# Kernel optimization log

Measured on AMD Instinct MI355X. Metric: run time of the kernel, lower is better.

## Reference

```python
import jax, jax.numpy as jnp
import numpy as np

E = 4096      # num hyperedges (events)
H1 = 512      # hidden1
H2 = 128      # hidden2 (latent)
NA, NK, NV = 8192, 4096, 1024   # nodes per type: author / keyword / venue
NNZ = 131072  # nonzeros per incidence matrix
SCALE = 0.02  # weight init scale (keeps tanh/exp in sane range)


def setup_inputs() -> dict:
    key = jax.random.key(0)
    ks = iter(jax.random.split(key, 64))
    nrm = lambda shape, s=SCALE: jax.random.normal(next(ks), shape, jnp.float32) * s
    inp = {}
    for t, N in (("a", NA), ("k", NK), ("v", NV)):
        inp["rows_" + t] = jax.random.randint(next(ks), (NNZ,), 0, N, dtype=jnp.int32)
        inp["cols_" + t] = jax.random.randint(next(ks), (NNZ,), 0, E, dtype=jnp.int32)
        inp["vals_" + t] = jax.random.uniform(next(ks), (NNZ,), jnp.float32)
        inp["Wn_" + t] = nrm((E, H1));  inp["bn_" + t] = jnp.zeros((H1,), jnp.float32)
        inp["Wzm_" + t] = nrm((H1, H2)); inp["bzm_" + t] = jnp.zeros((H2,), jnp.float32)
        inp["Wzs_" + t] = nrm((H1, H2)); inp["bzs_" + t] = jnp.zeros((H2,), jnp.float32)
        inp["We_" + t] = nrm((N, H1));  inp["be_" + t] = jnp.zeros((H1,), jnp.float32)
        inp["eps_" + t] = jax.random.normal(next(ks), (N, H2), jnp.float32)
    inp["Watt"] = nrm((H1, H1 // 2)); inp["batt"] = jnp.zeros((H1 // 2,), jnp.float32)
    inp["uatt"] = nrm((H1 // 2,), 0.1)
    inp["Wem"] = nrm((H1, H2)); inp["bem"] = jnp.zeros((H2,), jnp.float32)
    inp["Wes"] = nrm((H1, H2)); inp["bes"] = jnp.zeros((H2,), jnp.float32)
    inp["eps_e"] = jax.random.normal(next(ks), (E, H2), jnp.float32)
    return inp


def _type_branch(rows, cols, vals, N, Wn, bn, Wzm, bzm, Wzs, bzs, We, be, eps):
    # node encoder: tanh(sparse_inc @ Wn + bn);  sparse_inc is [N, E] in COO form
    h = jnp.tanh(jax.ops.segment_sum(vals[:, None] * Wn[cols], rows, num_segments=N) + bn)
    zm = h @ Wzm + bzm
    zs = h @ Wzs + bzs
    z = zm + eps * jnp.exp(zs)          # reparameterization
    # edge encoder: tanh(sparse_inc^T @ We + be) -> [E, H1]
    e = jnp.tanh(jax.ops.segment_sum(vals[:, None] * We[rows], cols, num_segments=E) + be)
    return zm, z, e


def _forward(rows_a, cols_a, vals_a, Wn_a, bn_a, Wzm_a, bzm_a, Wzs_a, bzs_a, We_a, be_a, eps_a,
             rows_k, cols_k, vals_k, Wn_k, bn_k, Wzm_k, bzm_k, Wzs_k, bzs_k, We_k, be_k, eps_k,
             rows_v, cols_v, vals_v, Wn_v, bn_v, Wzm_v, bzm_v, Wzs_v, bzs_v, We_v, be_v, eps_v,
             Watt, batt, uatt, Wem, bem, Wes, bes, eps_e):
    zm_a, z_a, e_a = _type_branch(rows_a, cols_a, vals_a, NA, Wn_a, bn_a, Wzm_a, bzm_a, Wzs_a, bzs_a, We_a, be_a, eps_a)
    zm_k, z_k, e_k = _type_branch(rows_k, cols_k, vals_k, NK, Wn_k, bn_k, Wzm_k, bzm_k, Wzs_k, bzs_k, We_k, be_k, eps_k)
    zm_v, z_v, e_v = _type_branch(rows_v, cols_v, vals_v, NV, Wn_v, bn_v, Wzm_v, bzm_v, Wzs_v, bzs_v, We_v, be_v, eps_v)

    # HyperedgeAttention over node types: [E, T=3, H1]
    edge_embeds = jnp.stack([e_a, e_k, e_v], axis=1)
    u = jnp.tanh(jnp.einsum('eth,hd->etd', edge_embeds, Watt) + batt)
    scores = jnp.einsum('etd,d->et', u, uatt)
    alphas = jax.nn.softmax(scores, axis=1)                  # [E, T]
    edge_embed = jnp.einsum('et,eth->eh', alphas, edge_embeds)  # [E, H1]

    zem = edge_embed @ Wem + bem
    zes = edge_embed @ Wes + bes
    ze = zem + eps_e * jnp.exp(zes)

    # InnerDecoder: z_node @ z_edge^T per type, flattened (sampled and mean variants)
    recon = jnp.concatenate([
        (z_a @ ze.T).ravel(), (z_k @ ze.T).ravel(), (z_v @ ze.T).ravel(),
        (zm_a @ zem.T).ravel(), (zm_k @ zem.T).ravel(), (zm_v @ zem.T).ravel(),
    ])
    return recon


def reference(rows_a, cols_a, vals_a, rows_k, cols_k, vals_k, rows_v, cols_v, vals_v,
              Wn_a, bn_a, Wzm_a, bzm_a, Wzs_a, bzs_a, We_a, be_a, eps_a,
              Wn_k, bn_k, Wzm_k, bzm_k, Wzs_k, bzs_k, We_k, be_k, eps_k,
              Wn_v, bn_v, Wzm_v, bzm_v, Wzs_v, bzs_v, We_v, be_v, eps_v,
              Watt, batt, uatt, Wem, bem, Wes, bes, eps_e):
    return _forward(rows_a, cols_a, vals_a, Wn_a, bn_a, Wzm_a, bzm_a, Wzs_a, bzs_a, We_a, be_a, eps_a,
                    rows_k, cols_k, vals_k, Wn_k, bn_k, Wzm_k, bzm_k, Wzs_k, bzs_k, We_k, be_k, eps_k,
                    rows_v, cols_v, vals_v, Wn_v, bn_v, Wzm_v, bzm_v, Wzs_v, bzs_v, We_v, be_v, eps_v,
                    Watt, batt, uatt, Wem, bem, Wes, bes, eps_e)
```

## Files before the change

### kernel.cpp

```cpp
#include <hip/hip_runtime.h>
#include <hip/hip_bf16.h>

#define NE   4096
#define D1   512
#define D2   128
#define NNZV 131072
#define MTOT 13312

typedef __attribute__((ext_vector_type(8))) short bf16x8;
typedef __attribute__((ext_vector_type(4))) float f32x4;

struct Params {
  const int*   rows[3]; const int* cols[3]; const float* vals[3];
  const float* Wn[3];  const float* bn[3];
  const float* Wzm[3]; const float* bzm[3];
  const float* Wzs[3]; const float* bzs[3];
  const float* We[3];  const float* be[3];
  const float* eps[3];
  const float* Watt; const float* batt; const float* uatt;
  const float* Wem;  const float* bem;  const float* Wes; const float* bes;
  const float* eps_e;
  int* cnt[6]; int* ptr[6]; int* cur[6]; int2* spair[6];
  __hip_bfloat16* Wbf[6];
  __hip_bfloat16* hbf[3];
  __hip_bfloat16* Wzmt[3];
  __hip_bfloat16* Wzst[3];
  float* e[3];
  __hip_bfloat16* Zbf; __hip_bfloat16* Zmbf; __hip_bfloat16* zebf; __hip_bfloat16* zembf;
  float* out;
  int rowbase[3];
  int n8pre[7];
  int ndw;
};

__device__ __forceinline__ float bf2f(short s) {
  return __uint_as_float((unsigned)(unsigned short)s << 16);
}

__device__ __forceinline__ int nseg_of(int sub) {
  if (sub & 1) return NE;
  int t = sub >> 1;
  return t == 0 ? 8192 : (t == 1 ? 4096 : 1024);
}

__global__ void prep_kernel(Params p) {
  int i = blockIdx.x * blockDim.x + threadIdx.x;
  if (i < p.ndw) { ((int*)p.cnt[0])[i] = 0; return; }
  int c = i - p.ndw;
  if (c < p.n8pre[6]) {
    int s = 0;
#pragma unroll
    for (int k = 1; k < 6; ++k) if (c >= p.n8pre[k]) s = k;
    int off8 = c - p.n8pre[s];
    int t = s >> 1;
    const float* src = (s & 1) ? p.We[t] : p.Wn[t];
    __hip_bfloat16* dst = p.Wbf[s];
    const float4 a = *(const float4*)&src[(size_t)off8 * 8];
    const float4 b = *(const float4*)&src[(size_t)off8 * 8 + 4];
    bf16x8 o;
    o[0] = (short)__bfloat16_as_ushort(__float2bfloat16(a.x));
    o[1] = (short)__bfloat16_as_ushort(__float2bfloat16(a.y));
    o[2] = (short)__bfloat16_as_ushort(__float2bfloat16(a.z));
    o[3] = (short)__bfloat16_as_ushort(__float2bfloat16(a.w));
    o[4] = (short)__bfloat16_as_ushort(__float2bfloat16(b.x));
    o[5] = (short)__bfloat16_as_ushort(__float2bfloat16(b.y));
    o[6] = (short)__bfloat16_as_ushort(__float2bfloat16(b.z));
    o[7] = (short)__bfloat16_as_ushort(__float2bfloat16(b.w));
    *(bf16x8*)&dst[(size_t)off8 * 8] = o;
    return;
  }
  int c2 = c - p.n8pre[6];
  if (c2 >= 6 * D1 * D2) return;
  int m = c2 >> 16;
  int e = c2 & 65535;
  int t = m >> 1;
  const float* src = (m & 1) ? p.Wzs[t] : p.Wzm[t];
  __hip_bfloat16* dst = (m & 1) ? p.Wzst[t] : p.Wzmt[t];
  int k = e >> 7, n = e & 127;
  dst[n * D1 + k] = __float2bfloat16(src[e]);
}

__global__ void hist_kernel(Params p) {
  int i = blockIdx.x * blockDim.x + threadIdx.x;
  if (i >= 6 * NNZV) return;
  int sub = i >> 17, idx = i & (NNZV - 1);
  int type = sub >> 1, dir = sub & 1;
  int seg = dir ? p.cols[type][idx] : p.rows[type][idx];
  atomicAdd(&p.cnt[sub][seg], 1);
}

__global__ __launch_bounds__(1024) void scan_kernel(Params p) {
  int sub = blockIdx.x;
  int n = nseg_of(sub);
  const int* cnt = p.cnt[sub];
  int* ptr = p.ptr[sub];
  int* cur = p.cur[sub];
  __shared__ int lds[1024];
  int tid = threadIdx.x;
  int per = (n + 1023) >> 10;
  int base = tid * per;
  int s = 0;
  for (int q = 0; q < per; ++q) { int ix = base + q; if (ix < n) s += cnt[ix]; }
  lds[tid] = s;
  __syncthreads();
  for (int off = 1; off < 1024; off <<= 1) {
    int v = (tid >= off) ? lds[tid - off] : 0;
    __syncthreads();
    lds[tid] += v;
    __syncthreads();
  }
  int prefix = (tid == 0) ? 0 : lds[tid - 1];
  for (int q = 0; q < per; ++q) {
    int ix = base + q;
    if (ix < n) { int c = cnt[ix]; ptr[ix] = prefix; cur[ix] = prefix; prefix += c; }
  }
  if (tid == 1023) ptr[n] = lds[1023];
}

__global__ void scatter_kernel(Params p) {
  int i = blockIdx.x * blockDim.x + threadIdx.x;
  if (i >= 6 * NNZV) return;
  int sub = i >> 17, idx = i & (NNZV - 1);
  int type = sub >> 1, dir = sub & 1;
  int seg = dir ? p.cols[type][idx] : p.rows[type][idx];
  int oth = dir ? p.rows[type][idx] : p.cols[type][idx];
  int pos = atomicAdd(&p.cur[sub][seg], 1);
  p.spair[sub][pos] = make_int2(oth, __float_as_int(p.vals[type][idx]));
}

__global__ __launch_bounds__(128) void spmm_kernel(Params p) {
  int g = blockIdx.x * 2 + (threadIdx.x >> 6);
  int sub, seg;
  if      (g <  8192) { sub = 0; seg = g;         }
  else if (g < 12288) { sub = 1; seg = g - 8192;  }
  else if (g < 16384) { sub = 2; seg = g - 12288; }
  else if (g < 20480) { sub = 3; seg = g - 16384; }
  else if (g < 21504) { sub = 4; seg = g - 20480; }
  else                { sub = 5; seg = g - 21504; }
  int type = sub >> 1, dir = sub & 1;
  const __hip_bfloat16* W = p.Wbf[sub];
  const float* bias = dir ? p.be[type] : p.bn[type];
  const int*  ptr  = p.ptr[sub];
  const int2* pair = p.spair[sub];
  int lane = threadIdx.x & 63;
  int c0 = lane * 8;
  float acc[8];
#pragma unroll
  for (int j = 0; j < 8; ++j) acc[j] = 0.f;
  int q0 = ptr[seg], q1 = ptr[seg + 1];
  int q = q0;
  for (; q + 4 <= q1; q += 4) {
    int2 pr0 = pair[q], pr1 = pair[q + 1], pr2 = pair[q + 2], pr3 = pair[q + 3];
    const bf16x8 w0 = *(const bf16x8*)(W + (size_t)pr0.x * D1 + c0);
    const bf16x8 w1 = *(const bf16x8*)(W + (size_t)pr1.x * D1 + c0);
    const bf16x8 w2 = *(const bf16x8*)(W + (size_t)pr2.x * D1 + c0);
    const bf16x8 w3 = *(const bf16x8*)(W + (size_t)pr3.x * D1 + c0);
    float v0 = __int_as_float(pr0.y), v1 = __int_as_float(pr1.y);
    float v2 = __int_as_float(pr2.y), v3 = __int_as_float(pr3.y);
#pragma unroll
    for (int j = 0; j < 8; ++j)
      acc[j] += v0 * bf2f(w0[j]) + v1 * bf2f(w1[j]) + v2 * bf2f(w2[j]) + v3 * bf2f(w3[j]);
  }
  for (; q < q1; ++q) {
    int2 pr = pair[q];
    const bf16x8 wv = *(const bf16x8*)(W + (size_t)pr.x * D1 + c0);
    float v = __int_as_float(pr.y);
#pragma unroll
    for (int j = 0; j < 8; ++j) acc[j] += v * bf2f(wv[j]);
  }
  const float4 b0 = *(const float4*)&bias[c0];
  const float4 b1 = *(const float4*)&bias[c0 + 4];
  float r[8];
  r[0] = tanhf(acc[0] + b0.x); r[1] = tanhf(acc[1] + b0.y);
  r[2] = tanhf(acc[2] + b0.z); r[3] = tanhf(acc[3] + b0.w);
  r[4] = tanhf(acc[4] + b1.x); r[5] = tanhf(acc[5] + b1.y);
  r[6] = tanhf(acc[6] + b1.z); r[7] = tanhf(acc[7] + b1.w);
  if (dir) {
    float4 o0 = {r[0], r[1], r[2], r[3]};
    float4 o1 = {r[4], r[5], r[6], r[7]};
    *(float4*)&p.e[type][(size_t)seg * D1 + c0]     = o0;
    *(float4*)&p.e[type][(size_t)seg * D1 + c0 + 4] = o1;
  } else {
    bf16x8 ob;
#pragma unroll
    for (int j = 0; j < 8; ++j) ob[j] = (short)__bfloat16_as_ushort(__float2bfloat16(r[j]));
    *(bf16x8*)&p.hbf[type][(size_t)seg * D1 + c0] = ob;
  }
}

__global__ __launch_bounds__(128) void zmzs_kernel(Params p) {
  int b = blockIdx.x;
  int type, blk;
  if      (b < 256) { type = 0; blk = b;       }
  else if (b < 384) { type = 1; blk = b - 256; }
  else              { type = 2; blk = b - 384; }
  int row0 = blk * 32;
  const __hip_bfloat16* A  = p.hbf[type];
  const __hip_bfloat16* Bm = p.Wzmt[type];
  const __hip_bfloat16* Bs = p.Wzst[type];
  int wid = threadIdx.x >> 6, lane = threadIdx.x & 63;
  int rloc = lane & 15, kg = lane >> 4;
  int mrow = row0 + wid * 16 + rloc;
  f32x4 accm[8], accs[8];
  f32x4 zero = {0.f, 0.f, 0.f, 0.f};
#pragma unroll
  for (int nf = 0; nf < 8; ++nf) { accm[nf] = zero; accs[nf] = zero; }
  for (int kk = 0; kk < 16; ++kk) {
    bf16x8 a = *(const bf16x8*)(A + (size_t)mrow * D1 + kk * 32 + kg * 8);
#pragma unroll
    for (int nf = 0; nf < 8; ++nf) {
      int ncol = nf * 16 + rloc;
      bf16x8 bm = *(const bf16x8*)(Bm + (size_t)ncol * D1 + kk * 32 + kg * 8);
      accm[nf] = __builtin_amdgcn_mfma_f32_16x16x32_bf16(a, bm, accm[nf], 0, 0, 0);
      bf16x8 bs = *(const bf16x8*)(Bs + (size_t)ncol * D1 + kk * 32 + kg * 8);
      accs[nf] = __builtin_amdgcn_mfma_f32_16x16x32_bf16(a, bs, accs[nf], 0, 0, 0);
    }
  }
  int base = p.rowbase[type];
  const float* eps = p.eps[type];
  const float* bzm = p.bzm[type];
  const float* bzs = p.bzs[type];
  int rbase = row0 + wid * 16 + kg * 4;
#pragma unroll
  for (int nf = 0; nf < 8; ++nf) {
    int col = nf * 16 + rloc;
    float bm = bzm[col], bs = bzs[col];
#pragma unroll
    for (int jj = 0; jj < 4; ++jj) {
      int row = rbase + jj;
      float zm = accm[nf][jj] + bm;
      float zs = accs[nf][jj] + bs;
      float ep = eps[(size_t)row * D2 + col];
      float z  = zm + ep * expf(zs);
      size_t oi = (size_t)(base + row) * D2 + col;
      p.Zmbf[oi] = __float2bfloat16(zm);
      p.Zbf[oi]  = __float2bfloat16(z);
    }
  }
}

__global__ __launch_bounds__(256) void scorecomb_kernel(Params p) {
  __shared__ __align__(16) float em[24 * D1];
  __shared__ float sc[24];
  __shared__ float alpha[8][3];
  int e0 = blockIdx.x * 8;
  int tid = threadIdx.x;
  for (int i4 = tid; i4 < 24 * (D1 / 4); i4 += 256) {
    int r = i4 >> 7, h4 = i4 & 127;
    int el = r / 3, t = r - el * 3;
    ((float4*)em)[i4] = ((const float4*)(p.e[t] + (size_t)(e0 + el) * D1))[h4];
  }
  __syncthreads();
  int lane = tid & 63, w = tid >> 6;
  {
    int d0 = lane * 4;
    float acc[6][4];
#pragma unroll
    for (int r = 0; r < 6; ++r) { acc[r][0]=acc[r][1]=acc[r][2]=acc[r][3]=0.f; }
    for (int hh = 0; hh < D1; hh += 4) {
      float4 w0 = *(const float4*)&p.Watt[(size_t)(hh+0) * 256 + d0];
      float4 w1 = *(const float4*)&p.Watt[(size_t)(hh+1) * 256 + d0];
      float4 w2 = *(const float4*)&p.Watt[(size_t)(hh+2) * 256 + d0];
      float4 w3 = *(const float4*)&p.Watt[(size_t)(hh+3) * 256 + d0];
#pragma unroll
      for (int r = 0; r < 6; ++r) {
        const float4 ev = *(const float4*)&em[(w * 6 + r) * D1 + hh];
        acc[r][0] += ev.x*w0.x + ev.y*w1.x + ev.z*w2.x + ev.w*w3.x;
        acc[r][1] += ev.x*w0.y + ev.y*w1.y + ev.z*w2.y + ev.w*w3.y;
        acc[r][2] += ev.x*w0.z + ev.y*w1.z + ev.z*w2.z + ev.w*w3.z;
        acc[r][3] += ev.x*w0.w + ev.y*w1.w + ev.z*w2.w + ev.w*w3.w;
      }
    }
    const float4 u4 = *(const float4*)&p.uatt[d0];
    const float4 b4 = *(const float4*)&p.batt[d0];
#pragma unroll
    for (int r = 0; r < 6; ++r) {
      float s = u4.x * tanhf(acc[r][0] + b4.x) + u4.y * tanhf(acc[r][1] + b4.y)
              + u4.z * tanhf(acc[r][2] + b4.z) + u4.w * tanhf(acc[r][3] + b4.w);
#pragma unroll
      for (int off = 32; off > 0; off >>= 1) s += __shfl_down(s, off, 64);
      if (lane == 0) sc[w * 6 + r] = s;
    }
  }
  __syncthreads();
  if (tid < 8) {
    float s0 = sc[tid * 3 + 0], s1 = sc[tid * 3 + 1], s2 = sc[tid * 3 + 2];
    float m = fmaxf(s0, fmaxf(s1, s2));
    float a0 = expf(s0 - m), a1 = expf(s1 - m), a2 = expf(s2 - m);
    float inv = 1.f / (a0 + a1 + a2);
    alpha[tid][0] = a0 * inv; alpha[tid][1] = a1 * inv; alpha[tid][2] = a2 * inv;
  }
  __syncthreads();
  float4 ve[4];
#pragma unroll
  for (int k = 0; k < 4; ++k) {
    int i4 = tid + k * 256;
    int el = i4 >> 7, h4 = i4 & 127;
    float4 va = ((const float4*)em)[(el * 3 + 0) * 128 + h4];
    float4 vk = ((const float4*)em)[(el * 3 + 1) * 128 + h4];
    float4 vv = ((const float4*)em)[(el * 3 + 2) * 128 + h4];
    float a0 = alpha[el][0], a1 = alpha[el][1], a2 = alpha[el][2];
    ve[k].x = a0*va.x + a1*vk.x + a2*vv.x;
    ve[k].y = a0*va.y + a1*vk.y + a2*vv.y;
    ve[k].z = a0*va.z + a1*vk.z + a2*vv.z;
    ve[k].w = a0*va.w + a1*vk.w + a2*vv.w;
  }
  __syncthreads();
#pragma unroll
  for (int k = 0; k < 4; ++k)
    ((float4*)em)[tid + k * 256] = ve[k];
  __syncthreads();
  int jp = tid & 63, eg = tid >> 6;
  int j = jp * 2;
  float am[2][2], as[2][2];
#pragma unroll
  for (int r = 0; r < 2; ++r) { am[r][0]=am[r][1]=as[r][0]=as[r][1]=0.f; }
  for (int hh = 0; hh < D1; hh += 4) {
    float2 wm[4], ws[4];
#pragma unroll
    for (int q = 0; q < 4; ++q) {
      wm[q] = *(const float2*)&p.Wem[(size_t)(hh + q) * D2 + j];
      ws[q] = *(const float2*)&p.Wes[(size_t)(hh + q) * D2 + j];
    }
#pragma unroll
    for (int r = 0; r < 2; ++r) {
      const float4 ev = *(const float4*)&em[(eg * 2 + r) * D1 + hh];
      am[r][0] += ev.x*wm[0].x + ev.y*wm[1].x + ev.z*wm[2].x + ev.w*wm[3].x;
      am[r][1] += ev.x*wm[0].y + ev.y*wm[1].y + ev.z*wm[2].y + ev.w*wm[3].y;
      as[r][0] += ev.x*ws[0].x + ev.y*ws[1].x + ev.z*ws[2].x + ev.w*ws[3].x;
      as[r][1] += ev.x*ws[0].y + ev.y*ws[1].y + ev.z*ws[2].y + ev.w*ws[3].y;
    }
  }
  float bm0 = p.bem[j], bm1 = p.bem[j+1], bs0 = p.bes[j], bs1 = p.bes[j+1];
#pragma unroll
  for (int r = 0; r < 2; ++r) {
    int e = e0 + eg * 2 + r;
    float zm0 = am[r][0] + bm0, zm1 = am[r][1] + bm1;
    float zs0 = as[r][0] + bs0, zs1 = as[r][1] + bs1;
    float e0v = p.eps_e[(size_t)e * D2 + j], e1v = p.eps_e[(size_t)e * D2 + j + 1];
    float z0 = zm0 + e0v * expf(zs0), z1 = zm1 + e1v * expf(zs1);
    size_t oi = (size_t)e * D2 + j;
    p.zembf[oi]   = __float2bfloat16(zm0); p.zembf[oi+1] = __float2bfloat16(zm1);
    p.zebf[oi]    = __float2bfloat16(z0);  p.zebf[oi+1]  = __float2bfloat16(z1);
  }
}

#define DT_N 128
__global__ __launch_bounds__(256) void decode_kernel(Params p) {
  __shared__ __align__(16) float cs[64][DT_N + 4];
  int which = blockIdx.z;
  const __hip_bfloat16* A = which ? p.Zmbf  : p.Zbf;
  const __hip_bfloat16* B = which ? p.zembf : p.zebf;
  float* C = p.out + (size_t)which * MTOT * NE;
  int n0 = blockIdx.x * DT_N;
  int m0 = blockIdx.y * 64;
  int wid  = threadIdx.x >> 6;
  int lane = threadIdx.x & 63;
  int rloc = lane & 15;
  int kg   = lane >> 4;
  int mrow = m0 + wid * 16 + rloc;
  bf16x8 a[4];
#pragma unroll
  for (int kk = 0; kk < 4; ++kk)
    a[kk] = *(const bf16x8*)(A + (size_t)mrow * D2 + kk * 32 + kg * 8);
  f32x4 acc[DT_N / 16];
  f32x4 zero = {0.f, 0.f, 0.f, 0.f};
#pragma unroll
  for (int nf = 0; nf < DT_N / 16; ++nf) acc[nf] = zero;
#pragma unroll
  for (int nf = 0; nf < DT_N / 16; ++nf) {
    int ncol = n0 + nf * 16 + rloc;
#pragma unroll
    for (int kk = 0; kk < 4; ++kk) {
      bf16x8 bv = *(const bf16x8*)(B + (size_t)ncol * D2 + kk * 32 + kg * 8);
      acc[nf] = __builtin_amdgcn_mfma_f32_16x16x32_bf16(a[kk], bv, acc[nf], 0, 0, 0);
    }
  }
#pragma unroll
  for (int nf = 0; nf < DT_N / 16; ++nf)
#pragma unroll
    for (int jj = 0; jj < 4; ++jj)
      cs[wid * 16 + kg * 4 + jj][nf * 16 + rloc] = acc[nf][jj];
  __syncthreads();
  int r_l  = threadIdx.x >> 5;
  int c4   = (threadIdx.x & 31) * 4;
#pragma unroll
  for (int it = 0; it < 8; ++it) {
    int r = it * 8 + r_l;
    f32x4 v = *(const f32x4*)&cs[r][c4];
    __builtin_nontemporal_store(v, (f32x4*)&C[(size_t)(m0 + r) * NE + n0 + c4]);
  }
}

extern "C" void kernel_launch(void* const* d_in, const int* in_sizes, int n_in,
                              void* d_out, int out_size, void* d_ws, size_t ws_size,
                              hipStream_t stream) {
  (void)in_sizes; (void)n_in; (void)out_size; (void)ws_size;
  static const int Ns[3] = {8192, 4096, 1024};
  static const int NsegH[6] = {8192, 4096, 4096, 4096, 1024, 4096};

  Params p;
  for (int t = 0; t < 3; ++t) {
    const int o = t * 12;
    p.rows[t] = (const int*)d_in[o + 0];
    p.cols[t] = (const int*)d_in[o + 1];
    p.vals[t] = (const float*)d_in[o + 2];
    p.Wn[t]   = (const float*)d_in[o + 3];
    p.bn[t]   = (const float*)d_in[o + 4];
    p.Wzm[t]  = (const float*)d_in[o + 5];
    p.bzm[t]  = (const float*)d_in[o + 6];
    p.Wzs[t]  = (const float*)d_in[o + 7];
    p.bzs[t]  = (const float*)d_in[o + 8];
    p.We[t]   = (const float*)d_in[o + 9];
    p.be[t]   = (const float*)d_in[o + 10];
    p.eps[t]  = (const float*)d_in[o + 11];
  }
  p.Watt  = (const float*)d_in[36];
  p.batt  = (const float*)d_in[37];
  p.uatt  = (const float*)d_in[38];
  p.Wem   = (const float*)d_in[39];
  p.bem   = (const float*)d_in[40];
  p.Wes   = (const float*)d_in[41];
  p.bes   = (const float*)d_in[42];
  p.eps_e = (const float*)d_in[43];
  p.out = (float*)d_out;
  p.rowbase[0] = 0; p.rowbase[1] = 8192; p.rowbase[2] = 12288;

  char* ws = (char*)d_ws;
  size_t off = 0;
  auto alloc = [&](size_t bytes) -> char* {
    char* r = ws + off;
    off += (bytes + 255) & ~(size_t)255;
    return r;
  };
  for (int s = 0; s < 6; ++s) p.cnt[s] = (int*)alloc((size_t)(NsegH[s] + 1) * 4);
  size_t cnt_bytes = off;
  for (int s = 0; s < 6; ++s) {
    p.ptr[s]   = (int*)alloc((size_t)(NsegH[s] + 1) * 4);
    p.cur[s]   = (int*)alloc((size_t)(NsegH[s] + 1) * 4);
    p.spair[s] = (int2*)alloc((size_t)NNZV * 8);
  }
  for (int s = 0; s < 6; ++s) {
    int t = s >> 1;
    int nrows = (s & 1) ? Ns[t] : NE;
    p.Wbf[s] = (__hip_bfloat16*)alloc((size_t)nrows * D1 * 2);
  }
  for (int t = 0; t < 3; ++t) p.hbf[t]  = (__hip_bfloat16*)alloc((size_t)Ns[t] * D1 * 2);
  for (int t = 0; t < 3; ++t) p.Wzmt[t] = (__hip_bfloat16*)alloc((size_t)D2 * D1 * 2);
  for (int t = 0; t < 3; ++t) p.Wzst[t] = (__hip_bfloat16*)alloc((size_t)D2 * D1 * 2);
  for (int t = 0; t < 3; ++t) p.e[t] = (float*)alloc((size_t)NE * D1 * 4);
  p.Zbf    = (__hip_bfloat16*)alloc((size_t)MTOT * D2 * 2);
  p.Zmbf   = (__hip_bfloat16*)alloc((size_t)MTOT * D2 * 2);
  p.zebf   = (__hip_bfloat16*)alloc((size_t)NE * D2 * 2);
  p.zembf  = (__hip_bfloat16*)alloc((size_t)NE * D2 * 2);

  p.ndw = (int)(cnt_bytes >> 2);
  p.n8pre[0] = 0;
  for (int s = 0; s < 6; ++s) {
    int t = s >> 1;
    int nrows = (s & 1) ? Ns[t] : NE;
    p.n8pre[s + 1] = p.n8pre[s] + nrows * (D1 / 8);
  }

  int prep_threads = p.ndw + p.n8pre[6] + 6 * D1 * D2;
  prep_kernel     <<<(prep_threads + 255) / 256, 256, 0, stream>>>(p);
  hist_kernel     <<<(6 * NNZV + 255) / 256, 256, 0, stream>>>(p);
  scan_kernel     <<<6, 1024, 0, stream>>>(p);
  scatter_kernel  <<<(6 * NNZV + 255) / 256, 256, 0, stream>>>(p);
  spmm_kernel     <<<12800, 128, 0, stream>>>(p);
  zmzs_kernel     <<<416, 128, 0, stream>>>(p);
  scorecomb_kernel<<<512, 256, 0, stream>>>(p);
  decode_kernel   <<<dim3(NE / DT_N, 208, 2), 256, 0, stream>>>(p);
}
```

Before: 607.4 us.

## Move attention scoring and edge latent projection onto bf16 MFMA kernels

Replaces the fp32 scalar scorecomb kernel with three kernels: an MFMA bf16 GEMM for the attention scores with a fused tanh/u-dot reduction, a softmax-weighted combine, and an MFMA GEMM for the zem/zes projection. Edge encoder outputs are now stored as bf16 instead of fp32, halving that traffic. Watt, Wem and Wes are pre-transposed to bf16 in prep. This adds two launches and lowers precision for the attention path.

```diff
diff --git a/kernel.cpp b/kernel.cpp
--- a/kernel.cpp
+++ b/kernel.cpp
@@ -23,9 +23,14 @@
   int* cnt[6]; int* ptr[6]; int* cur[6]; int2* spair[6];
   __hip_bfloat16* Wbf[6];
   __hip_bfloat16* hbf[3];
+  __hip_bfloat16* ebf[3];
+  __hip_bfloat16* eebf;
   __hip_bfloat16* Wzmt[3];
   __hip_bfloat16* Wzst[3];
-  float* e[3];
+  __hip_bfloat16* Wattt;
+  __hip_bfloat16* Wemt;
+  __hip_bfloat16* West;
+  float* scores;
   __hip_bfloat16* Zbf; __hip_bfloat16* Zmbf; __hip_bfloat16* zebf; __hip_bfloat16* zembf;
   float* out;
   int rowbase[3];
@@ -69,15 +74,30 @@
     *(bf16x8*)&dst[(size_t)off8 * 8] = o;
     return;
   }
-  int c2 = c - p.n8pre[6];
-  if (c2 >= 6 * D1 * D2) return;
-  int m = c2 >> 16;
-  int e = c2 & 65535;
-  int t = m >> 1;
-  const float* src = (m & 1) ? p.Wzs[t] : p.Wzm[t];
-  __hip_bfloat16* dst = (m & 1) ? p.Wzst[t] : p.Wzmt[t];
-  int k = e >> 7, n = e & 127;
-  dst[n * D1 + k] = __float2bfloat16(src[e]);
+  int cz = c - p.n8pre[6];
+  if (cz < 6 * D1 * D2) {
+    int m = cz >> 16, e = cz & 65535;
+    int t = m >> 1;
+    const float* src = (m & 1) ? p.Wzs[t] : p.Wzm[t];
+    __hip_bfloat16* dst = (m & 1) ? p.Wzst[t] : p.Wzmt[t];
+    int k = e >> 7, n = e & 127;
+    dst[n * D1 + k] = __float2bfloat16(src[e]);
+    return;
+  }
+  int cz2 = cz - 6 * D1 * D2;
+  if (cz2 < D1 * 256) {
+    int k = cz2 >> 8, n = cz2 & 255;
+    p.Wattt[n * D1 + k] = __float2bfloat16(p.Watt[(size_t)k * 256 + n]);
+    return;
+  }
+  int cz3 = cz2 - D1 * 256;
+  if (cz3 < 2 * D1 * D2) {
+    int m = cz3 >> 16, e = cz3 & 65535;
+    const float* src = m ? p.Wes : p.Wem;
+    __hip_bfloat16* dst = m ? p.West : p.Wemt;
+    int k = e >> 7, n = e & 127;
+    dst[n * D1 + k] = __float2bfloat16(src[e]);
+  }
 }
 
 __global__ void hist_kernel(Params p) {
@@ -175,17 +195,11 @@
   r[2] = tanhf(acc[2] + b0.z); r[3] = tanhf(acc[3] + b0.w);
   r[4] = tanhf(acc[4] + b1.x); r[5] = tanhf(acc[5] + b1.y);
   r[6] = tanhf(acc[6] + b1.z); r[7] = tanhf(acc[7] + b1.w);
-  if (dir) {
-    float4 o0 = {r[0], r[1], r[2], r[3]};
-    float4 o1 = {r[4], r[5], r[6], r[7]};
-    *(float4*)&p.e[type][(size_t)seg * D1 + c0]     = o0;
-    *(float4*)&p.e[type][(size_t)seg * D1 + c0 + 4] = o1;
-  } else {
-    bf16x8 ob;
-#pragma unroll
-    for (int j = 0; j < 8; ++j) ob[j] = (short)__bfloat16_as_ushort(__float2bfloat16(r[j]));
-    *(bf16x8*)&p.hbf[type][(size_t)seg * D1 + c0] = ob;
-  }
+  bf16x8 ob;
+#pragma unroll
+  for (int j = 0; j < 8; ++j) ob[j] = (short)__bfloat16_as_ushort(__float2bfloat16(r[j]));
+  __hip_bfloat16* outp = dir ? p.ebf[type] : p.hbf[type];
+  *(bf16x8*)&outp[(size_t)seg * D1 + c0] = ob;
 }
 
 __global__ __launch_bounds__(128) void zmzs_kernel(Params p) {
@@ -239,109 +253,116 @@
   }
 }
 
-__global__ __launch_bounds__(256) void scorecomb_kernel(Params p) {
-  __shared__ __align__(16) float em[24 * D1];
-  __shared__ float sc[24];
-  __shared__ float alpha[8][3];
-  int e0 = blockIdx.x * 8;
-  int tid = threadIdx.x;
-  for (int i4 = tid; i4 < 24 * (D1 / 4); i4 += 256) {
-    int r = i4 >> 7, h4 = i4 & 127;
-    int el = r / 3, t = r - el * 3;
-    ((float4*)em)[i4] = ((const float4*)(p.e[t] + (size_t)(e0 + el) * D1))[h4];
-  }
-  __syncthreads();
-  int lane = tid & 63, w = tid >> 6;
-  {
-    int d0 = lane * 4;
-    float acc[6][4];
-#pragma unroll
-    for (int r = 0; r < 6; ++r) { acc[r][0]=acc[r][1]=acc[r][2]=acc[r][3]=0.f; }
-    for (int hh = 0; hh < D1; hh += 4) {
-      float4 w0 = *(const float4*)&p.Watt[(size_t)(hh+0) * 256 + d0];
-      float4 w1 = *(const float4*)&p.Watt[(size_t)(hh+1) * 256 + d0];
-      float4 w2 = *(const float4*)&p.Watt[(size_t)(hh+2) * 256 + d0];
-      float4 w3 = *(const float4*)&p.Watt[(size_t)(hh+3) * 256 + d0];
-#pragma unroll
-      for (int r = 0; r < 6; ++r) {
-        const float4 ev = *(const float4*)&em[(w * 6 + r) * D1 + hh];
-        acc[r][0] += ev.x*w0.x + ev.y*w1.x + ev.z*w2.x + ev.w*w3.x;
-        acc[r][1] += ev.x*w0.y + ev.y*w1.y + ev.z*w2.y + ev.w*w3.y;
-        acc[r][2] += ev.x*w0.z + ev.y*w1.z + ev.z*w2.z + ev.w*w3.z;
-        acc[r][3] += ev.x*w0.w + ev.y*w1.w + ev.z*w2.w + ev.w*w3.w;
-      }
-    }
-    const float4 u4 = *(const float4*)&p.uatt[d0];
-    const float4 b4 = *(const float4*)&p.batt[d0];
-#pragma unroll
-    for (int r = 0; r < 6; ++r) {
-      float s = u4.x * tanhf(acc[r][0] + b4.x) + u4.y * tanhf(acc[r][1] + b4.y)
-              + u4.z * tanhf(acc[r][2] + b4.z) + u4.w * tanhf(acc[r][3] + b4.w);
-#pragma unroll
-      for (int off = 32; off > 0; off >>= 1) s += __shfl_down(s, off, 64);
-      if (lane == 0) sc[w * 6 + r] = s;
-    }
-  }
-  __syncthreads();
-  if (tid < 8) {
-    float s0 = sc[tid * 3 + 0], s1 = sc[tid * 3 + 1], s2 = sc[tid * 3 + 2];
-    float m = fmaxf(s0, fmaxf(s1, s2));
-    float a0 = expf(s0 - m), a1 = expf(s1 - m), a2 = expf(s2 - m);
-    float inv = 1.f / (a0 + a1 + a2);
-    alpha[tid][0] = a0 * inv; alpha[tid][1] = a1 * inv; alpha[tid][2] = a2 * inv;
-  }
-  __syncthreads();
-  float4 ve[4];
-#pragma unroll
-  for (int k = 0; k < 4; ++k) {
-    int i4 = tid + k * 256;
-    int el = i4 >> 7, h4 = i4 & 127;
-    float4 va = ((const float4*)em)[(el * 3 + 0) * 128 + h4];
-    float4 vk = ((const float4*)em)[(el * 3 + 1) * 128 + h4];
-    float4 vv = ((const float4*)em)[(el * 3 + 2) * 128 + h4];
-    float a0 = alpha[el][0], a1 = alpha[el][1], a2 = alpha[el][2];
-    ve[k].x = a0*va.x + a1*vk.x + a2*vv.x;
-    ve[k].y = a0*va.y + a1*vk.y + a2*vv.y;
-    ve[k].z = a0*va.z + a1*vk.z + a2*vv.z;
-    ve[k].w = a0*va.w + a1*vk.w + a2*vv.w;
-  }
-  __syncthreads();
-#pragma unroll
-  for (int k = 0; k < 4; ++k)
-    ((float4*)em)[tid + k * 256] = ve[k];
-  __syncthreads();
-  int jp = tid & 63, eg = tid >> 6;
-  int j = jp * 2;
-  float am[2][2], as[2][2];
-#pragma unroll
-  for (int r = 0; r < 2; ++r) { am[r][0]=am[r][1]=as[r][0]=as[r][1]=0.f; }
-  for (int hh = 0; hh < D1; hh += 4) {
-    float2 wm[4], ws[4];
-#pragma unroll
-    for (int q = 0; q < 4; ++q) {
-      wm[q] = *(const float2*)&p.Wem[(size_t)(hh + q) * D2 + j];
-      ws[q] = *(const float2*)&p.Wes[(size_t)(hh + q) * D2 + j];
-    }
-#pragma unroll
-    for (int r = 0; r < 2; ++r) {
-      const float4 ev = *(const float4*)&em[(eg * 2 + r) * D1 + hh];
-      am[r][0] += ev.x*wm[0].x + ev.y*wm[1].x + ev.z*wm[2].x + ev.w*wm[3].x;
-      am[r][1] += ev.x*wm[0].y + ev.y*wm[1].y + ev.z*wm[2].y + ev.w*wm[3].y;
-      as[r][0] += ev.x*ws[0].x + ev.y*ws[1].x + ev.z*ws[2].x + ev.w*ws[3].x;
-      as[r][1] += ev.x*ws[0].y + ev.y*ws[1].y + ev.z*ws[2].y + ev.w*ws[3].y;
-    }
-  }
-  float bm0 = p.bem[j], bm1 = p.bem[j+1], bs0 = p.bes[j], bs1 = p.bes[j+1];
-#pragma unroll
-  for (int r = 0; r < 2; ++r) {
-    int e = e0 + eg * 2 + r;
-    float zm0 = am[r][0] + bm0, zm1 = am[r][1] + bm1;
-    float zs0 = as[r][0] + bs0, zs1 = as[r][1] + bs1;
-    float e0v = p.eps_e[(size_t)e * D2 + j], e1v = p.eps_e[(size_t)e * D2 + j + 1];
-    float z0 = zm0 + e0v * expf(zs0), z1 = zm1 + e1v * expf(zs1);
-    size_t oi = (size_t)e * D2 + j;
-    p.zembf[oi]   = __float2bfloat16(zm0); p.zembf[oi+1] = __float2bfloat16(zm1);
-    p.zebf[oi]    = __float2bfloat16(z0);  p.zebf[oi+1]  = __float2bfloat16(z1);
+__global__ __launch_bounds__(256) void scores_kernel(Params p) {
+  int wtile = blockIdx.x * 4 + (threadIdx.x >> 6);
+  int t = wtile >> 8;
+  int tile = wtile & 255;
+  const __hip_bfloat16* A = p.ebf[t];
+  const __hip_bfloat16* B = p.Wattt;
+  int lane = threadIdx.x & 63;
+  int rloc = lane & 15, kg = lane >> 4;
+  int mrow = tile * 16 + rloc;
+  f32x4 acc[16];
+  f32x4 zero = {0.f, 0.f, 0.f, 0.f};
+#pragma unroll
+  for (int nf = 0; nf < 16; ++nf) acc[nf] = zero;
+  for (int kk = 0; kk < 16; ++kk) {
+    bf16x8 a = *(const bf16x8*)(A + (size_t)mrow * D1 + kk * 32 + kg * 8);
+#pragma unroll
+    for (int nf = 0; nf < 16; ++nf) {
+      int ncol = nf * 16 + rloc;
+      bf16x8 bv = *(const bf16x8*)(B + (size_t)ncol * D1 + kk * 32 + kg * 8);
+      acc[nf] = __builtin_amdgcn_mfma_f32_16x16x32_bf16(a, bv, acc[nf], 0, 0, 0);
+    }
+  }
+  float part[4] = {0.f, 0.f, 0.f, 0.f};
+#pragma unroll
+  for (int nf = 0; nf < 16; ++nf) {
+    int col = nf * 16 + rloc;
+    float ua = p.uatt[col], ba = p.batt[col];
+#pragma unroll
+    for (int jj = 0; jj < 4; ++jj)
+      part[jj] += ua * tanhf(acc[nf][jj] + ba);
+  }
+#pragma unroll
+  for (int off = 1; off < 16; off <<= 1) {
+#pragma unroll
+    for (int jj = 0; jj < 4; ++jj)
+      part[jj] += __shfl_xor(part[jj], off, 64);
+  }
+  if (rloc == 0) {
+#pragma unroll
+    for (int jj = 0; jj < 4; ++jj) {
+      int e = tile * 16 + kg * 4 + jj;
+      p.scores[e * 3 + t] = part[jj];
+    }
+  }
+}
+
+__global__ __launch_bounds__(256) void combine_kernel(Params p) {
+  int e = blockIdx.x * 4 + (threadIdx.x >> 6);
+  int lane = threadIdx.x & 63;
+  float s0 = p.scores[e * 3 + 0];
+  float s1 = p.scores[e * 3 + 1];
+  float s2 = p.scores[e * 3 + 2];
+  float m = fmaxf(s0, fmaxf(s1, s2));
+  float a0 = expf(s0 - m), a1 = expf(s1 - m), a2 = expf(s2 - m);
+  float inv = 1.f / (a0 + a1 + a2);
+  a0 *= inv; a1 *= inv; a2 *= inv;
+  int c0 = lane * 8;
+  const bf16x8 va = *(const bf16x8*)(p.ebf[0] + (size_t)e * D1 + c0);
+  const bf16x8 vk = *(const bf16x8*)(p.ebf[1] + (size_t)e * D1 + c0);
+  const bf16x8 vv = *(const bf16x8*)(p.ebf[2] + (size_t)e * D1 + c0);
+  bf16x8 o;
+#pragma unroll
+  for (int j = 0; j < 8; ++j) {
+    float v = a0 * bf2f(va[j]) + a1 * bf2f(vk[j]) + a2 * bf2f(vv[j]);
+    o[j] = (short)__bfloat16_as_ushort(__float2bfloat16(v));
+  }
+  *(bf16x8*)&p.eebf[(size_t)e * D1 + c0] = o;
+}
+
+__global__ __launch_bounds__(128) void zemzs_kernel(Params p) {
+  int row0 = blockIdx.x * 32;
+  const __hip_bfloat16* A  = p.eebf;
+  const __hip_bfloat16* Bm = p.Wemt;
+  const __hip_bfloat16* Bs = p.West;
+  int wid = threadIdx.x >> 6, lane = threadIdx.x & 63;
+  int rloc = lane & 15, kg = lane >> 4;
+  int mrow = row0 + wid * 16 + rloc;
+  f32x4 accm[8], accs[8];
+  f32x4 zero = {0.f, 0.f, 0.f, 0.f};
+#pragma unroll
+  for (int nf = 0; nf < 8; ++nf) { accm[nf] = zero; accs[nf] = zero; }
+  for (int kk = 0; kk < 16; ++kk) {
+    bf16x8 a = *(const bf16x8*)(A + (size_t)mrow * D1 + kk * 32 + kg * 8);
+#pragma unroll
+    for (int nf = 0; nf < 8; ++nf) {
+      int ncol = nf * 16 + rloc;
+      bf16x8 bm = *(const bf16x8*)(Bm + (size_t)ncol * D1 + kk * 32 + kg * 8);
+      accm[nf] = __builtin_amdgcn_mfma_f32_16x16x32_bf16(a, bm, accm[nf], 0, 0, 0);
+      bf16x8 bs = *(const bf16x8*)(Bs + (size_t)ncol * D1 + kk * 32 + kg * 8);
+      accs[nf] = __builtin_amdgcn_mfma_f32_16x16x32_bf16(a, bs, accs[nf], 0, 0, 0);
+    }
+  }
+  const float* bem = p.bem;
+  const float* bes = p.bes;
+  int rbase = row0 + wid * 16 + kg * 4;
+#pragma unroll
+  for (int nf = 0; nf < 8; ++nf) {
+    int col = nf * 16 + rloc;
+    float bm = bem[col], bs = bes[col];
+#pragma unroll
+    for (int jj = 0; jj < 4; ++jj) {
+      int row = rbase + jj;
+      float zm = accm[nf][jj] + bm;
+      float zs = accs[nf][jj] + bs;
+      float ep = p.eps_e[(size_t)row * D2 + col];
+      float z  = zm + ep * expf(zs);
+      size_t oi = (size_t)row * D2 + col;
+      p.zembf[oi] = __float2bfloat16(zm);
+      p.zebf[oi]  = __float2bfloat16(z);
+    }
   }
 }
 
@@ -446,9 +467,14 @@
     p.Wbf[s] = (__hip_bfloat16*)alloc((size_t)nrows * D1 * 2);
   }
   for (int t = 0; t < 3; ++t) p.hbf[t]  = (__hip_bfloat16*)alloc((size_t)Ns[t] * D1 * 2);
+  for (int t = 0; t < 3; ++t) p.ebf[t]  = (__hip_bfloat16*)alloc((size_t)NE * D1 * 2);
+  p.eebf = (__hip_bfloat16*)alloc((size_t)NE * D1 * 2);
   for (int t = 0; t < 3; ++t) p.Wzmt[t] = (__hip_bfloat16*)alloc((size_t)D2 * D1 * 2);
   for (int t = 0; t < 3; ++t) p.Wzst[t] = (__hip_bfloat16*)alloc((size_t)D2 * D1 * 2);
-  for (int t = 0; t < 3; ++t) p.e[t] = (float*)alloc((size_t)NE * D1 * 4);
+  p.Wattt = (__hip_bfloat16*)alloc((size_t)256 * D1 * 2);
+  p.Wemt  = (__hip_bfloat16*)alloc((size_t)D2 * D1 * 2);
+  p.West  = (__hip_bfloat16*)alloc((size_t)D2 * D1 * 2);
+  p.scores = (float*)alloc((size_t)NE * 3 * 4);
   p.Zbf    = (__hip_bfloat16*)alloc((size_t)MTOT * D2 * 2);
   p.Zmbf   = (__hip_bfloat16*)alloc((size_t)MTOT * D2 * 2);
   p.zebf   = (__hip_bfloat16*)alloc((size_t)NE * D2 * 2);
@@ -462,13 +488,15 @@
     p.n8pre[s + 1] = p.n8pre[s] + nrows * (D1 / 8);
   }
 
-  int prep_threads = p.ndw + p.n8pre[6] + 6 * D1 * D2;
-  prep_kernel     <<<(prep_threads + 255) / 256, 256, 0, stream>>>(p);
-  hist_kernel     <<<(6 * NNZV + 255) / 256, 256, 0, stream>>>(p);
-  scan_kernel     <<<6, 1024, 0, stream>>>(p);
-  scatter_kernel  <<<(6 * NNZV + 255) / 256, 256, 0, stream>>>(p);
-  spmm_kernel     <<<12800, 128, 0, stream>>>(p);
-  zmzs_kernel     <<<416, 128, 0, stream>>>(p);
-  scorecomb_kernel<<<512, 256, 0, stream>>>(p);
-  decode_kernel   <<<dim3(NE / DT_N, 208, 2), 256, 0, stream>>>(p);
-}
+  int prep_threads = p.ndw + p.n8pre[6] + 6 * D1 * D2 + D1 * 256 + 2 * D1 * D2;
+  prep_kernel    <<<(prep_threads + 255) / 256, 256, 0, stream>>>(p);
+  hist_kernel    <<<(6 * NNZV + 255) / 256, 256, 0, stream>>>(p);
+  scan_kernel    <<<6, 1024, 0, stream>>>(p);
+  scatter_kernel <<<(6 * NNZV + 255) / 256, 256, 0, stream>>>(p);
+  spmm_kernel    <<<12800, 128, 0, stream>>>(p);
+  zmzs_kernel    <<<416, 128, 0, stream>>>(p);
+  scores_kernel  <<<192, 256, 0, stream>>>(p);
+  combine_kernel <<<1024, 256, 0, stream>>>(p);
+  zemzs_kernel   <<<128, 128, 0, stream>>>(p);
+  decode_kernel  <<<dim3(NE / DT_N, 208, 2), 256, 0, stream>>>(p);
+}
```

Result: faster. 556.6 us (-8.4%).
